# Kernel optimization log

Measured on AMD Instinct MI355X. Metric: run time of the kernel, lower is better.

The kernel has to match this reference:

```python
import jax, jax.numpy as jnp
import numpy as np

B, T, D, H = 2, 2048, 768, 12
HS = D // H           # head_size = 64
FF = 4 * D            # feed_forward_multiplier = 4 -> hidden 3072
HALF = FF // 2        # SwiGLU halves hidden -> 1536
EPS = 1e-8


def rmsnorm(x, scale):
    # RMSNorm with p=-1: full-dim L2 norm / sqrt(d), then x/(rms+eps)*scale
    d = x.shape[-1]
    rms = jnp.linalg.norm(x, axis=-1, keepdims=True) * (d ** -0.5)
    return scale * (x / (rms + EPS))


def setup_inputs() -> dict:
    key = jax.random.key(0)
    ks = jax.random.split(key, 12)
    s = 0.02
    return {
        "x":  jax.random.normal(ks[0], (B, T, D), dtype=jnp.float32),
        "Wq": jax.random.normal(ks[1], (H, D, HS), dtype=jnp.float32) * s,
        "Wk": jax.random.normal(ks[2], (H, D, HS), dtype=jnp.float32) * s,
        "Wv": jax.random.normal(ks[3], (H, D, HS), dtype=jnp.float32) * s,
        "Wo": jax.random.normal(ks[4], (D, D), dtype=jnp.float32) * s,
        "bo": jnp.zeros((D,), dtype=jnp.float32),
        "W1": jax.random.normal(ks[5], (D, FF), dtype=jnp.float32) * s,
        "b1": jnp.zeros((FF,), dtype=jnp.float32),
        "W2": jax.random.normal(ks[6], (HALF, D), dtype=jnp.float32) * s,
        "b2": jnp.zeros((D,), dtype=jnp.float32),
        "g1": jnp.ones((D,), dtype=jnp.float32),
        "g2": jnp.ones((D,), dtype=jnp.float32),
    }


def reference(x, Wq, Wk, Wv, Wo, bo, W1, b1, W2, b2, g1, g2):
    Bx, Tx, Dx = x.shape
    # --- Multi-head causal attention (pre-RMSNorm, residual) ---
    h = rmsnorm(x, g1)
    q = jnp.einsum('btd,hdk->bhtk', h, Wq)
    k = jnp.einsum('btd,hdk->bhtk', h, Wk)
    v = jnp.einsum('btd,hdk->bhtk', h, Wv)
    # NOTE: original scales by C**-0.5 where C = embed_dim (not head_size)
    scores = jnp.einsum('bhtk,bhsk->bhts', q, k) * (Dx ** -0.5)
    causal = jnp.tril(jnp.ones((Tx, Tx), dtype=bool))
    scores = jnp.where(causal, scores, -jnp.inf)
    wei = jax.nn.softmax(scores, axis=-1)
    attn = jnp.einsum('bhts,bhsk->bhtk', wei, v)
    attn = attn.transpose(0, 2, 1, 3).reshape(Bx, Tx, Dx)  # concat heads
    x = x + attn @ Wo + bo
    # --- SwiGLU FFN (pre-RMSNorm, residual) ---
    h2 = rmsnorm(x, g2)
    u = h2 @ W1 + b1
    a, gate = jnp.split(u, 2, axis=-1)  # chunk: first half = value, second = gate
    x = x + (jax.nn.silu(gate) * a) @ W2 + b2
    return x
```

## Files before the change

### kernel.cpp

```cpp
#include <hip/hip_runtime.h>
#include <math.h>

#define TDIM 2048
#define DDIM 768
#define NH   12
#define NROWS 4096
#define EPSV 1e-8f
#define SCALE 0.03608439182435161f

typedef __bf16 bf16_t;
typedef bf16_t bf16x8 __attribute__((ext_vector_type(8)));
typedef bf16_t bf16x4 __attribute__((ext_vector_type(4)));
typedef bf16_t bf16x2 __attribute__((ext_vector_type(2)));
typedef float  floatx4 __attribute__((ext_vector_type(4)));

__device__ __forceinline__ void glds16(const bf16_t* g, bf16_t* l) {
    __builtin_amdgcn_global_load_lds(
        (const __attribute__((address_space(1))) void*)g,
        (__attribute__((address_space(3))) void*)l, 16, 0, 0);
}

__global__ __launch_bounds__(256) void pack_rms(
    const float* __restrict__ Wq, const float* __restrict__ Wk,
    const float* __restrict__ Wv, const float* __restrict__ Wo,
    const float* __restrict__ W1, const float* __restrict__ W2,
    bf16_t* __restrict__ qkvw, bf16_t* __restrict__ wo,
    bf16_t* __restrict__ w1, bf16_t* __restrict__ w2,
    const float* __restrict__ x, const float* __restrict__ g1,
    bf16_t* __restrict__ hout)
{
    __shared__ float Ts[64][65];
    __shared__ float red[4];
    __shared__ float tot;
    int bid = blockIdx.x;
    int tid = threadIdx.x;

    if (bid >= 1440) {
        int row = bid - 1440;
        const float* xr = x + (size_t)row * DDIM;
        float v0 = xr[tid], v1 = xr[tid + 256], v2 = xr[tid + 512];
        float s = v0*v0 + v1*v1 + v2*v2;
        #pragma unroll
        for (int off = 32; off > 0; off >>= 1)
            s += __shfl_down(s, off, 64);
        if ((tid & 63) == 0) red[tid >> 6] = s;
        __syncthreads();
        if (tid == 0) tot = red[0] + red[1] + red[2] + red[3];
        __syncthreads();
        float rms = sqrtf(tot * (1.0f / DDIM));
        float inv = 1.0f / (rms + EPSV);
        bf16_t* orow = hout + (size_t)row * DDIM;
        orow[tid]       = (bf16_t)(g1[tid]       * v0 * inv);
        orow[tid + 256] = (bf16_t)(g1[tid + 256] * v1 * inv);
        orow[tid + 512] = (bf16_t)(g1[tid + 512] * v2 * inv);
        return;
    }

    const float* src; bf16_t* dst;
    int srcld, dstld, k0, n0;
    int remap = 0;
    if (bid < 144) {
        int kx = bid % 12, nx = bid / 12;
        src = Wo; dst = wo; srcld = 768; dstld = 768; k0 = kx * 64; n0 = nx * 64;
    } else if (bid < 720) {
        int t = bid - 144; int kx = t % 12, nx = t / 12;
        src = W1; dst = w1; srcld = 3072; dstld = 768; k0 = kx * 64; n0 = nx * 64;
        remap = 1;
    } else if (bid < 1008) {
        int t = bid - 720; int kx = t % 24, nx = t / 24;
        src = W2; dst = w2; srcld = 768; dstld = 1536; k0 = kx * 64; n0 = nx * 64;
    } else {
        int t = bid - 1008; int kx = t % 12, y = t / 12;
        int sel = y / 12, h = y - sel * 12;
        src = ((sel == 0) ? Wq : (sel == 1) ? Wk : Wv) + (size_t)h * 768 * 64;
        dst = qkvw + (size_t)(sel * 768 + h * 64) * 768;
        srcld = 64; dstld = 768; k0 = kx * 64; n0 = 0;
    }
    int r = tid >> 2, c = (tid & 3) * 16;
    const float* s = src + (size_t)(k0 + r) * srcld + n0 + c;
    #pragma unroll
    for (int i = 0; i < 4; i++) {
        float4 t = *(const float4*)(s + i * 4);
        Ts[r][c + i*4 + 0] = t.x; Ts[r][c + i*4 + 1] = t.y;
        Ts[r][c + i*4 + 2] = t.z; Ts[r][c + i*4 + 3] = t.w;
    }
    __syncthreads();
    int n = tid >> 2, kk = (tid & 3) * 16;
    bf16x8 o0, o1;
    #pragma unroll
    for (int i = 0; i < 8; i++) {
        o0[i] = (bf16_t)Ts[kk + i][n];
        o1[i] = (bf16_t)Ts[kk + 8 + i][n];
    }
    int oc = n0 + n;
    if (remap) oc = (oc < 1536) ? (oc * 2) : ((oc - 1536) * 2 + 1);
    bf16_t* d = dst + (size_t)oc * dstld + k0 + kk;
    *(bf16x8*)d = o0;
    *(bf16x8*)(d + 8) = o1;
}

__global__ __launch_bounds__(256) void rmsnorm_bf(
    const float* __restrict__ x, const float* __restrict__ g,
    bf16_t* __restrict__ out)
{
    int row = blockIdx.x;
    int tid = threadIdx.x;
    const float* xr = x + (size_t)row * DDIM;
    float v0 = xr[tid], v1 = xr[tid + 256], v2 = xr[tid + 512];
    float s = v0*v0 + v1*v1 + v2*v2;
    #pragma unroll
    for (int off = 32; off > 0; off >>= 1)
        s += __shfl_down(s, off, 64);
    __shared__ float red[4];
    __shared__ float tot;
    if ((tid & 63) == 0) red[tid >> 6] = s;
    __syncthreads();
    if (tid == 0) tot = red[0] + red[1] + red[2] + red[3];
    __syncthreads();
    float rms = sqrtf(tot * (1.0f / DDIM));
    float inv = 1.0f / (rms + EPSV);
    bf16_t* orow = out + (size_t)row * DDIM;
    orow[tid]       = (bf16_t)(g[tid]       * v0 * inv);
    orow[tid + 256] = (bf16_t)(g[tid + 256] * v1 * inv);
    orow[tid + 512] = (bf16_t)(g[tid + 512] * v2 * inv);
}

template<int TM, int EPI>
__global__ __launch_bounds__(256) void gemm_bf16(
    const bf16_t* __restrict__ A, const bf16_t* __restrict__ BT, int K,
    float* __restrict__ Cf, bf16_t* __restrict__ Cb, int ldc,
    const float* __restrict__ bias, const float* __restrict__ resid, int gx,
    bf16_t* __restrict__ vtout)
{
    constexpr int MT = TM / 32;
    __shared__ bf16_t As0[TM][32], As1[TM][32];
    __shared__ bf16_t Bs0[128][32], Bs1[128][32];
    int tid = threadIdx.x;
    int wave = tid >> 6, lane = tid & 63;
    int lrow = lane & 15, quad = lane >> 4;
    int wm = wave >> 1, wn = wave & 1;

    int flat = blockIdx.x;
    int cpx = gridDim.x >> 3;
    int swz = (flat & 7) * cpx + (flat >> 3);
    int m0 = (swz / gx) * TM;
    int n0 = (swz % gx) * 128;

    int srow = lane >> 2, scol = (lane & 3) * 8;
    const bf16_t* Ag = A  + ((size_t)m0 + wave * (TM/4) + srow) * K + scol;
    const bf16_t* Bg = BT + ((size_t)n0 + wave * 32 + srow) * K + scol;

    floatx4 acc[MT][4];
    #pragma unroll
    for (int mt = 0; mt < MT; mt++)
        #pragma unroll
        for (int nt = 0; nt < 4; nt++)
            #pragma unroll
            for (int r = 0; r < 4; r++) acc[mt][nt][r] = 0.f;

    for (int k0 = 0; k0 < K; k0 += 64) {
        __syncthreads();
        #pragma unroll
        for (int i = 0; i < TM/64; i++) {
            glds16(Ag + (size_t)(i*16) * K + k0,      &As0[wave*(TM/4) + i*16][0]);
            glds16(Ag + (size_t)(i*16) * K + k0 + 32, &As1[wave*(TM/4) + i*16][0]);
        }
        #pragma unroll
        for (int i = 0; i < 2; i++) {
            glds16(Bg + (size_t)(i*16) * K + k0,      &Bs0[wave*32 + i*16][0]);
            glds16(Bg + (size_t)(i*16) * K + k0 + 32, &Bs1[wave*32 + i*16][0]);
        }
        __syncthreads();

        bf16x8 af0[MT], af1[MT], bf0[4], bf1[4];
        #pragma unroll
        for (int mt = 0; mt < MT; mt++) {
            af0[mt] = *(const bf16x8*)&As0[wm*(TM/2) + mt*16 + lrow][quad * 8];
            af1[mt] = *(const bf16x8*)&As1[wm*(TM/2) + mt*16 + lrow][quad * 8];
        }
        #pragma unroll
        for (int nt = 0; nt < 4; nt++) {
            bf0[nt] = *(const bf16x8*)&Bs0[wn*64 + nt*16 + lrow][quad * 8];
            bf1[nt] = *(const bf16x8*)&Bs1[wn*64 + nt*16 + lrow][quad * 8];
        }
        #pragma unroll
        for (int mt = 0; mt < MT; mt++)
            #pragma unroll
            for (int nt = 0; nt < 4; nt++) {
                acc[mt][nt] = __builtin_amdgcn_mfma_f32_16x16x32_bf16(
                    bf0[nt], af0[mt], acc[mt][nt], 0, 0, 0);
                acc[mt][nt] = __builtin_amdgcn_mfma_f32_16x16x32_bf16(
                    bf1[nt], af1[mt], acc[mt][nt], 0, 0, 0);
            }
    }

    int crow0 = m0 + wm * (TM/2);
    int ccol0 = n0 + wn * 64;
    #pragma unroll
    for (int mt = 0; mt < MT; mt++) {
        int row = crow0 + mt * 16 + lrow;
        #pragma unroll
        for (int nt = 0; nt < 4; nt++) {
            int col = ccol0 + nt * 16 + quad * 4;
            floatx4 a = acc[mt][nt];
            if constexpr (EPI == 1) {
                int c = col >> 1;
                float2 ba = *(const float2*)(bias + c);
                float2 bg = *(const float2*)(bias + 1536 + c);
                float a0 = a[0] + ba.x, g0 = a[1] + bg.x;
                float a1 = a[2] + ba.y, g1 = a[3] + bg.y;
                bf16x2 v;
                v[0] = (bf16_t)(a0 * (g0 / (1.0f + __expf(-g0))));
                v[1] = (bf16_t)(a1 * (g1 / (1.0f + __expf(-g1))));
                *(bf16x2*)(Cb + (size_t)row * ldc + c) = v;
            } else if constexpr (EPI == 2) {
                if (col < 1536) {
                    bf16x4 v;
                    v[0] = (bf16_t)a[0]; v[1] = (bf16_t)a[1];
                    v[2] = (bf16_t)a[2]; v[3] = (bf16_t)a[3];
                    *(bf16x4*)(Cb + (size_t)row * ldc + col) = v;
                } else {
                    int vcol = col - 1536;
                    int hh = vcol >> 6, d0 = vcol & 63;
                    int bb = row >> 11, tt = row & 2047;
                    bf16_t* vbase2 = vtout +
                        ((size_t)(bb * NH + hh) * 64 + d0) * TDIM + tt;
                    #pragma unroll
                    for (int r = 0; r < 4; r++)
                        vbase2[(size_t)r * TDIM] = (bf16_t)a[r];
                }
            } else {
                size_t off = (size_t)row * ldc + col;
                float4 bv = make_float4(0.f, 0.f, 0.f, 0.f);
                if (bias) bv = *(const float4*)(bias + col);
                float4 rs = make_float4(0.f, 0.f, 0.f, 0.f);
                if (resid) rs = *(const float4*)(resid + off);
                if (Cf) {
                    float4 v;
                    v.x = a[0] + bv.x + rs.x; v.y = a[1] + bv.y + rs.y;
                    v.z = a[2] + bv.z + rs.z; v.w = a[3] + bv.w + rs.w;
                    *(float4*)(Cf + off) = v;
                } else {
                    bf16x4 v;
                    v[0] = (bf16_t)(a[0] + bv.x + rs.x);
                    v[1] = (bf16_t)(a[1] + bv.y + rs.y);
                    v[2] = (bf16_t)(a[2] + bv.z + rs.z);
                    v[3] = (bf16_t)(a[3] + bv.w + rs.w);
                    *(bf16x4*)(Cb + off) = v;
                }
            }
        }
    }
}

__global__ __launch_bounds__(256) void attn_mfma(
    const bf16_t* __restrict__ qkv, const bf16_t* __restrict__ vt,
    bf16_t* __restrict__ o)
{
    const int QS = 2304;
    int bid = blockIdx.x;
    int c = bid & 255, slot = bid >> 8;
    int x = c & 31, g = c >> 5;
    int qt, bh;
    if (slot == 0)      { bh = g;      qt = x; }
    else if (slot == 1) { bh = 8 + g;  qt = (x + 16) & 31; }
    else                { bh = 16 + g; qt = (x < 16) ? (31 - 2 * x) : (62 - 2 * x); }
    int b = bh / NH, h = bh - b * NH;
    int tid = threadIdx.x;
    int wave = tid >> 6, lane = tid & 63;
    int lrow = lane & 15, quad = lane >> 4;

    __shared__ bf16_t Ks[2][64][72];
    __shared__ bf16_t Vts[2][64][72];
    __shared__ bf16_t Ps[4][16][72];

    size_t rbase = (size_t)b * TDIM;
    int q0 = qt * 64, qrow_w = q0 + wave * 16;

    const bf16_t* qp = qkv + (rbase + qrow_w + lrow) * QS + h * 64;
    bf16x8 qf[2];
    qf[0] = *(const bf16x8*)(qp + quad * 8);
    qf[1] = *(const bf16x8*)(qp + 32 + quad * 8);

    floatx4 o_acc[4];
    #pragma unroll
    for (int mt = 0; mt < 4; mt++)
        #pragma unroll
        for (int r = 0; r < 4; r++) o_acc[mt][r] = 0.f;
    float m_r = -INFINITY, l_r = 0.f;

    int srow = tid >> 2;
    int scol = (tid & 3) * 16;
    const bf16_t* kbase = qkv + (rbase + srow) * QS + 768 + h * 64 + scol;
    const bf16_t* vbase = vt + ((size_t)bh * 64 + srow) * TDIM + scol;

    bf16x8 kr0 = *(const bf16x8*)kbase;
    bf16x8 kr1 = *(const bf16x8*)(kbase + 8);
    bf16x8 vr0 = *(const bf16x8*)vbase;
    bf16x8 vr1 = *(const bf16x8*)(vbase + 8);
    *(bf16x8*)&Ks[0][srow][scol]      = kr0;
    *(bf16x8*)&Ks[0][srow][scol + 8]  = kr1;
    *(bf16x8*)&Vts[0][srow][scol]     = vr0;
    *(bf16x8*)&Vts[0][srow][scol + 8] = vr1;
    if (qt >= 1) {
        const bf16_t* kp = kbase + (size_t)64 * QS;
        const bf16_t* vp = vbase + 64;
        kr0 = *(const bf16x8*)kp;  kr1 = *(const bf16x8*)(kp + 8);
        vr0 = *(const bf16x8*)vp;  vr1 = *(const bf16x8*)(vp + 8);
    }
    asm volatile("s_waitcnt lgkmcnt(0)" ::: "memory");
    __builtin_amdgcn_s_barrier();

    for (int s = 0; s <= qt; s++) {
        int cur = s & 1;

        floatx4 sfrag[4];
        __builtin_amdgcn_s_setprio(1);
        #pragma unroll
        for (int nt = 0; nt < 4; nt++) {
            floatx4 a;
            #pragma unroll
            for (int r = 0; r < 4; r++) a[r] = 0.f;
            #pragma unroll
            for (int kf = 0; kf < 2; kf++) {
                bf16x8 afr = *(const bf16x8*)&Ks[cur][nt * 16 + lrow][kf * 32 + quad * 8];
                a = __builtin_amdgcn_mfma_f32_16x16x32_bf16(afr, qf[kf], a, 0, 0, 0);
            }
            sfrag[nt] = a;
        }
        __builtin_amdgcn_s_setprio(0);

        if (s < qt) {
            int nxt = cur ^ 1;
            *(bf16x8*)&Ks[nxt][srow][scol]      = kr0;
            *(bf16x8*)&Ks[nxt][srow][scol + 8]  = kr1;
            *(bf16x8*)&Vts[nxt][srow][scol]     = vr0;
            *(bf16x8*)&Vts[nxt][srow][scol + 8] = vr1;
        }

        if (s == qt) {
            int qg = qrow_w + lrow;
            #pragma unroll
            for (int nt = 0; nt < 4; nt++)
                #pragma unroll
                for (int r = 0; r < 4; r++) {
                    int kc = s * 64 + nt * 16 + quad * 4 + r;
                    sfrag[nt][r] = (kc > qg) ? -INFINITY : sfrag[nt][r] * SCALE;
                }
        } else {
            #pragma unroll
            for (int nt = 0; nt < 4; nt++)
                #pragma unroll
                for (int r = 0; r < 4; r++) sfrag[nt][r] *= SCALE;
        }

        float mx = sfrag[0][0];
        #pragma unroll
        for (int nt = 0; nt < 4; nt++)
            #pragma unroll
            for (int r = 0; r < 4; r++) mx = fmaxf(mx, sfrag[nt][r]);
        mx = fmaxf(mx, __shfl_xor(mx, 16, 64));
        mx = fmaxf(mx, __shfl_xor(mx, 32, 64));
        if (__any(mx > m_r + 8.0f)) {
            float mn = fmaxf(m_r, mx);
            float alpha = __expf(m_r - mn);
            m_r = mn;
            l_r *= alpha;
            #pragma unroll
            for (int mt = 0; mt < 4; mt++)
                #pragma unroll
                for (int r = 0; r < 4; r++) o_acc[mt][r] *= alpha;
        }

        float ls = 0.f;
        #pragma unroll
        for (int nt = 0; nt < 4; nt++) {
            bf16x4 pv;
            #pragma unroll
            for (int r = 0; r < 4; r++) {
                float p = __expf(sfrag[nt][r] - m_r);
                ls += p;
                pv[r] = (bf16_t)p;
            }
            *(bf16x4*)&Ps[wave][lrow][nt * 16 + quad * 4] = pv;
        }
        ls += __shfl_xor(ls, 16, 64);
        ls += __shfl_xor(ls, 32, 64);
        l_r += ls;

        __builtin_amdgcn_s_setprio(1);
        #pragma unroll
        for (int kf = 0; kf < 2; kf++) {
            bf16x8 pfr = *(const bf16x8*)&Ps[wave][lrow][kf * 32 + quad * 8];
            #pragma unroll
            for (int mt = 0; mt < 4; mt++) {
                bf16x8 vfr = *(const bf16x8*)&Vts[cur][mt * 16 + lrow][kf * 32 + quad * 8];
                o_acc[mt] = __builtin_amdgcn_mfma_f32_16x16x32_bf16(vfr, pfr, o_acc[mt], 0, 0, 0);
            }
        }
        __builtin_amdgcn_s_setprio(0);

        if (s + 2 <= qt) {
            const bf16_t* kp = kbase + (size_t)(s + 2) * 64 * QS;
            const bf16_t* vp = vbase + (size_t)(s + 2) * 64;
            kr0 = *(const bf16x8*)kp;  kr1 = *(const bf16x8*)(kp + 8);
            vr0 = *(const bf16x8*)vp;  vr1 = *(const bf16x8*)(vp + 8);
        }

        asm volatile("s_waitcnt lgkmcnt(0)" ::: "memory");
        __builtin_amdgcn_s_barrier();
    }

    float inv = 1.0f / l_r;
    size_t rb = (rbase + qrow_w + lrow) * DDIM + h * 64;
    #pragma unroll
    for (int mt = 0; mt < 4; mt++) {
        bf16x4 ov;
        #pragma unroll
        for (int r = 0; r < 4; r++) ov[r] = (bf16_t)(o_acc[mt][r] * inv);
        *(bf16x4*)(o + rb + mt * 16 + quad * 4) = ov;
    }
}

extern "C" void kernel_launch(void* const* d_in, const int* in_sizes, int n_in,
                              void* d_out, int out_size, void* d_ws, size_t ws_size,
                              hipStream_t stream) {
    const float* x  = (const float*)d_in[0];
    const float* Wq = (const float*)d_in[1];
    const float* Wk = (const float*)d_in[2];
    const float* Wv = (const float*)d_in[3];
    const float* Wo = (const float*)d_in[4];
    const float* bo = (const float*)d_in[5];
    const float* W1 = (const float*)d_in[6];
    const float* b1 = (const float*)d_in[7];
    const float* W2 = (const float*)d_in[8];
    const float* b2 = (const float*)d_in[9];
    const float* g1 = (const float*)d_in[10];
    const float* g2 = (const float*)d_in[11];
    float* out = (float*)d_out;
    char* ws = (char*)d_ws;

    bf16_t* qkvw_bt = (bf16_t*)(ws);
    bf16_t* wo_bt   = (bf16_t*)(ws + 3538944);
    bf16_t* w1_bt   = (bf16_t*)(ws + 4718592);
    bf16_t* w2_bt   = (bf16_t*)(ws + 9437184);
    bf16_t* h_bf    = (bf16_t*)(ws + 11796480);
    bf16_t* qkv     = (bf16_t*)(ws + 18087936);
    bf16_t* attn_bf = (bf16_t*)(ws + 36962304);
    bf16_t* sw_bf   = (bf16_t*)(ws + 68419584);
    bf16_t* vt      = (bf16_t*)(ws + 81002496);

    pack_rms<<<5536, 256, 0, stream>>>(Wq, Wk, Wv, Wo, W1, W2,
                                       qkvw_bt, wo_bt, w1_bt, w2_bt,
                                       x, g1, h_bf);

    gemm_bf16<128, 2><<<576, 256, 0, stream>>>(
        h_bf, qkvw_bt, 768, nullptr, qkv, 2304, nullptr, nullptr, 18, vt);

    attn_mfma<<<768, 256, 0, stream>>>(qkv, vt, attn_bf);

    gemm_bf16<64, 0><<<384, 256, 0, stream>>>(
        attn_bf, wo_bt, 768, out, nullptr, 768, bo, x, 6, nullptr);

    rmsnorm_bf<<<NROWS, 256, 0, stream>>>(out, g2, h_bf);

    gemm_bf16<128, 1><<<768, 256, 0, stream>>>(
        h_bf, w1_bt, 768, nullptr, sw_bf, 1536, b1, nullptr, 24, nullptr);

    gemm_bf16<64, 0><<<384, 256, 0, stream>>>(
        sw_bf, w2_bt, 1536, out, nullptr, 768, b2, out, 6, nullptr);
}
```

Baseline: 252.9 us.

## Split K across two wave groups in output-projection GEMMs with LDS reduction

Adds a KS template parameter to the bf16 GEMM so each block runs 512 threads. Each half of the block handles half of the K range in its own LDS buffers, and the two partial accumulators are then summed through shared memory. It is applied to the two TM=64 GEMMs (Wo and W2), which launch only 384 blocks, to get more waves in flight and halve each wave's K loop. The cost is extra LDS traffic, two more barriers, and more shared memory per block, which may lower occupancy.

```diff
diff --git a/kernel.cpp b/kernel.cpp
--- a/kernel.cpp
+++ b/kernel.cpp
@@ -125,18 +125,25 @@
     orow[tid + 512] = (bf16_t)(g[tid + 512] * v2 * inv);
 }
 
-template<int TM, int EPI>
-__global__ __launch_bounds__(256) void gemm_bf16(
+template<int TM, int EPI, int KS>
+__global__ __launch_bounds__(KS * 256) void gemm_bf16(
     const bf16_t* __restrict__ A, const bf16_t* __restrict__ BT, int K,
     float* __restrict__ Cf, bf16_t* __restrict__ Cb, int ldc,
     const float* __restrict__ bias, const float* __restrict__ resid, int gx,
     bf16_t* __restrict__ vtout)
 {
     constexpr int MT = TM / 32;
-    __shared__ bf16_t As0[TM][32], As1[TM][32];
-    __shared__ bf16_t Bs0[128][32], Bs1[128][32];
+    constexpr int HB = TM * 128 + 16384;
+    __shared__ char lraw[KS * HB];
     int tid = threadIdx.x;
-    int wave = tid >> 6, lane = tid & 63;
+    int kh = tid >> 8;
+    int t2 = tid & 255;
+    char* hb = lraw + kh * HB;
+    auto As0 = (bf16_t(*)[32])(hb);
+    auto As1 = (bf16_t(*)[32])(hb + TM * 64);
+    auto Bs0 = (bf16_t(*)[32])(hb + TM * 128);
+    auto Bs1 = (bf16_t(*)[32])(hb + TM * 128 + 8192);
+    int wave = t2 >> 6, lane = t2 & 63;
     int lrow = lane & 15, quad = lane >> 4;
     int wm = wave >> 1, wn = wave & 1;
 
@@ -146,9 +153,10 @@
     int m0 = (swz / gx) * TM;
     int n0 = (swz % gx) * 128;
 
+    int K2 = K / KS;
     int srow = lane >> 2, scol = (lane & 3) * 8;
-    const bf16_t* Ag = A  + ((size_t)m0 + wave * (TM/4) + srow) * K + scol;
-    const bf16_t* Bg = BT + ((size_t)n0 + wave * 32 + srow) * K + scol;
+    const bf16_t* Ag = A  + ((size_t)m0 + wave * (TM/4) + srow) * K + kh * K2 + scol;
+    const bf16_t* Bg = BT + ((size_t)n0 + wave * 32 + srow) * K + kh * K2 + scol;
 
     floatx4 acc[MT][4];
     #pragma unroll
@@ -158,7 +166,7 @@
             #pragma unroll
             for (int r = 0; r < 4; r++) acc[mt][nt][r] = 0.f;
 
-    for (int k0 = 0; k0 < K; k0 += 64) {
+    for (int k0 = 0; k0 < K2; k0 += 64) {
         __syncthreads();
         #pragma unroll
         for (int i = 0; i < TM/64; i++) {
@@ -192,6 +200,30 @@
                 acc[mt][nt] = __builtin_amdgcn_mfma_f32_16x16x32_bf16(
                     bf1[nt], af1[mt], acc[mt][nt], 0, 0, 0);
             }
+    }
+
+    if constexpr (KS == 2) {
+        __syncthreads();
+        float* comb = (float*)lraw;
+        float* p = comb + (size_t)(wave * 64 + lane) * 33;
+        if (kh == 1) {
+            #pragma unroll
+            for (int mt = 0; mt < MT; mt++)
+                #pragma unroll
+                for (int nt = 0; nt < 4; nt++)
+                    #pragma unroll
+                    for (int r = 0; r < 4; r++)
+                        p[mt*16 + nt*4 + r] = acc[mt][nt][r];
+        }
+        __syncthreads();
+        if (kh == 1) return;
+        #pragma unroll
+        for (int mt = 0; mt < MT; mt++)
+            #pragma unroll
+            for (int nt = 0; nt < 4; nt++)
+                #pragma unroll
+                for (int r = 0; r < 4; r++)
+                    acc[mt][nt][r] += p[mt*16 + nt*4 + r];
     }
 
     int crow0 = m0 + wm * (TM/2);
@@ -454,19 +486,19 @@
                                        qkvw_bt, wo_bt, w1_bt, w2_bt,
                                        x, g1, h_bf);
 
-    gemm_bf16<128, 2><<<576, 256, 0, stream>>>(
+    gemm_bf16<128, 2, 1><<<576, 256, 0, stream>>>(
         h_bf, qkvw_bt, 768, nullptr, qkv, 2304, nullptr, nullptr, 18, vt);
 
     attn_mfma<<<768, 256, 0, stream>>>(qkv, vt, attn_bf);
 
-    gemm_bf16<64, 0><<<384, 256, 0, stream>>>(
+    gemm_bf16<64, 0, 2><<<384, 512, 0, stream>>>(
         attn_bf, wo_bt, 768, out, nullptr, 768, bo, x, 6, nullptr);
 
     rmsnorm_bf<<<NROWS, 256, 0, stream>>>(out, g2, h_bf);
 
-    gemm_bf16<128, 1><<<768, 256, 0, stream>>>(
+    gemm_bf16<128, 1, 1><<<768, 256, 0, stream>>>(
         h_bf, w1_bt, 768, nullptr, sw_bf, 1536, b1, nullptr, 24, nullptr);
 
-    gemm_bf16<64, 0><<<384, 256, 0, stream>>>(
+    gemm_bf16<64, 0, 2><<<384, 512, 0, stream>>>(
         sw_bf, w2_bt, 1536, out, nullptr, 768, b2, out, 6, nullptr);
 }
```

Result: no change. 251.4 us (-0.6%).
